# Performance work log

Hardware: AMD Instinct MI355X
Metric: run time of the kernel (lower is better)

The kernel has to match this reference:

```python
import jax, jax.numpy as jnp
import numpy as np
import math

B, S, HID, H, DH = 4, 1024, 1024, 16, 64  # batch, seq, hidden, heads, head_dim


def _rotate_half(x):
    x1, x2 = jnp.split(x, 2, axis=-1)
    return jnp.concatenate([-x2, x1], axis=-1)


def _apply_rope(t, freqs):
    # t: [B,H,S,DH], freqs: [S,rot_dim]; here rot_dim == DH so no pass-through part
    rot = freqs.shape[-1]
    cos_ = jnp.cos(freqs)[None, None, :, :].astype(t.dtype)
    sin_ = jnp.sin(freqs)[None, None, :, :].astype(t.dtype)
    t_rot, t_pass = t[..., :rot], t[..., rot:]
    t_rot = t_rot * cos_ + _rotate_half(t_rot) * sin_
    return jnp.concatenate([t_rot, t_pass], axis=-1)


def setup_inputs() -> dict:
    key = jax.random.key(0)
    ks = jax.random.split(key, 8)
    hidden_states = jax.random.normal(ks[0], (B, S, HID), dtype=jnp.float32)
    # additive mask: valid prefix of random length per batch row, -1e9 on padding
    lengths = jax.random.randint(ks[1], (B,), 3 * S // 4, S + 1)
    pos = jnp.arange(S)
    attention_mask = jnp.where(pos[None, :] < lengths[:, None], 0.0, -1e9)
    attention_mask = attention_mask.astype(jnp.float32)[:, None, None, :]  # [B,1,1,S]
    # rotary frequencies: standard RoPE angles, duplicated halves -> [S, DH]
    inv_freq = 1.0 / (10000.0 ** (jnp.arange(0, DH // 2, dtype=jnp.float32) / (DH // 2)))
    ang = pos.astype(jnp.float32)[:, None] * inv_freq[None, :]
    freqs = jnp.concatenate([ang, ang], axis=-1)  # [S, DH]
    sc = 0.02
    Wq = jax.random.normal(ks[2], (HID, HID), dtype=jnp.float32) * sc
    Wk = jax.random.normal(ks[3], (HID, HID), dtype=jnp.float32) * sc
    Wv = jax.random.normal(ks[4], (HID, HID), dtype=jnp.float32) * sc
    bq = jnp.zeros((HID,), dtype=jnp.float32)
    bk = jnp.zeros((HID,), dtype=jnp.float32)
    bv = jnp.zeros((HID,), dtype=jnp.float32)
    return dict(hidden_states=hidden_states, attention_mask=attention_mask, freqs=freqs,
                Wq=Wq, bq=bq, Wk=Wk, bk=bk, Wv=Wv, bv=bv)


def reference(hidden_states, attention_mask, freqs, Wq, bq, Wk, bk, Wv, bv):
    b, s, _ = hidden_states.shape
    # QKV projections -> [B,H,S,DH]
    q = (hidden_states @ Wq + bq).reshape(b, s, H, DH).transpose(0, 2, 1, 3)
    k = (hidden_states @ Wk + bk).reshape(b, s, H, DH).transpose(0, 2, 1, 3)
    v = (hidden_states @ Wv + bv).reshape(b, s, H, DH).transpose(0, 2, 1, 3)
    # inline RoPE on q and k (same freqs for both, as (rotary_pos_emb,)*2)
    q = _apply_rope(q, freqs)
    k = _apply_rope(k, freqs)
    scores = jnp.einsum('bhqd,bhkd->bhqk', q, k) / math.sqrt(DH)
    scores = scores + attention_mask  # additive mask broadcast over [B,H,S,S]
    probs = jax.nn.softmax(scores, axis=-1)
    # no_prob_mask filtering: zero out masked key columns
    probs = jnp.where(attention_mask < -1e-5, 0.0, probs)
    # dropout prob is 0.0 (eval) -> identity
    ctx = jnp.einsum('bhqk,bhkd->bhqd', probs, v)
    ctx = ctx.transpose(0, 2, 1, 3).reshape(b, s, H * DH)
    return ctx
```

## Files before the change

kernel.cpp:

```cpp
#include <hip/hip_runtime.h>
#include <hip/hip_bf16.h>
#include <cmath>

#define NB   4
#define NS   1024
#define NHID 1024
#define NH   16
#define NDH  64
#define QKV_PLANE (NB * NH * NS * NDH)

typedef __attribute__((ext_vector_type(8))) short bf16x8;
typedef __attribute__((ext_vector_type(4))) float f32x4;

typedef __attribute__((address_space(1))) const void gv_t;
typedef __attribute__((address_space(3))) void       lv_t;

__device__ __forceinline__ void gload16(const void* g, void* l) {
    __builtin_amdgcn_global_load_lds((gv_t*)g, (lv_t*)l, 16, 0, 0);
}

__device__ __forceinline__ unsigned short f2b(float f) {
    union { float f; unsigned int u; } v; v.f = f;
    unsigned int r = (v.u + 0x7fff + ((v.u >> 16) & 1)) >> 16;
    return (unsigned short)r;
}

__device__ __forceinline__ unsigned int f2b2(float a, float b) {
    __hip_bfloat162 h = __float22bfloat162_rn(make_float2(a, b));
    union { __hip_bfloat162 h; unsigned int u; } v; v.h = h;
    return v.u;
}

__device__ __forceinline__ float fexp2(float x) {
#if __has_builtin(__builtin_amdgcn_exp2f)
    return __builtin_amdgcn_exp2f(x);
#else
    return exp2f(x);
#endif
}

__global__ __launch_bounds__(256) void cast_hs_kernel(
    const float* __restrict__ hs, unsigned short* __restrict__ hsb)
{
    const int idx = (blockIdx.x * 256 + threadIdx.x) * 4;
    float4 v = *(const float4*)&hs[idx];
    ushort4 o;
    o.x = f2b(v.x); o.y = f2b(v.y); o.z = f2b(v.z); o.w = f2b(v.w);
    *(ushort4*)&hsb[idx] = o;
}

__global__ __launch_bounds__(256) void wt_prep_kernel(
    const float* __restrict__ Wq, const float* __restrict__ Wk,
    const float* __restrict__ Wv, unsigned short* __restrict__ wt)
{
    const int z = blockIdx.z;
    const float* __restrict__ W = (z == 0) ? Wq : (z == 1) ? Wk : Wv;
    __shared__ float t[64][65];
    const int k0 = blockIdx.x * 64, n0 = blockIdx.y * 64;
    const int tid = threadIdx.x;
    #pragma unroll
    for (int c = 0; c < 16; ++c) {
        const int flat = c * 256 + tid;
        const int r = flat >> 6, cc = flat & 63;
        t[r][cc] = W[(size_t)(k0 + r) * NHID + n0 + cc];
    }
    __syncthreads();
    #pragma unroll
    for (int c = 0; c < 16; ++c) {
        const int flat = c * 256 + tid;
        const int r = flat >> 6, cc = flat & 63;
        wt[(size_t)(z * 1024 + n0 + r) * NHID + k0 + cc] = f2b(t[cc][r]);
    }
}

__global__ __launch_bounds__(256) void fused_gemm_kernel(
    const unsigned short* __restrict__ hsb,
    const unsigned short* __restrict__ wt,
    const float* __restrict__ freqs,
    const float* __restrict__ bq, const float* __restrict__ bk,
    const float* __restrict__ bv,
    unsigned short* __restrict__ qkv)
{
    __shared__ short As[128 * 32];
    __shared__ short Bs[128 * 32];

    const int tid  = threadIdx.x;
    const int lane = tid & 63;
    const int wv   = __builtin_amdgcn_readfirstlane(tid >> 6);
    const bool vmode = (blockIdx.x >= 16);

    const unsigned short* Amat;
    const unsigned short* Bmat;
    int a_base, b_base, m0, n0, vb_ = 0;
    if (!vmode) {
        n0 = blockIdx.x * 128;
        m0 = blockIdx.y * 128;
        Amat = hsb;  a_base = m0;
        Bmat = wt;   b_base = n0;
    } else {
        m0  = (blockIdx.x - 16) * 128;
        vb_ = blockIdx.y >> 3;
        n0  = (blockIdx.y & 7) * 128;
        Amat = wt;   a_base = 2048 + m0;
        Bmat = hsb;  b_base = vb_ * 1024 + n0;
    }

    const int L0 = 2 * wv, L1 = 2 * wv + 1;
    const int r_in = lane >> 2;
    const int kc   = (lane & 3) * 8;
    const unsigned short* gA0 = Amat + (size_t)(a_base + L0 * 16 + r_in) * NHID + kc;
    const unsigned short* gA1 = Amat + (size_t)(a_base + L1 * 16 + r_in) * NHID + kc;
    const unsigned short* gB0 = Bmat + (size_t)(b_base + L0 * 16 + r_in) * NHID + kc;
    const unsigned short* gB1 = Bmat + (size_t)(b_base + L1 * 16 + r_in) * NHID + kc;
    short* lA0 = As + L0 * 512;
    short* lA1 = As + L1 * 512;
    short* lB0 = Bs + L0 * 512;
    short* lB1 = Bs + L1 * 512;

    const int R  = (wv & 1) * 64;
    const int CW = (wv >> 1) * 64;
    const int c0 = lane & 15;
    const int kg = (lane >> 4) * 8;
    int aoff[4], boff[4];
    #pragma unroll
    for (int i = 0; i < 4; ++i) aoff[i] = (R  + 16 * i + c0) * 32 + kg;
    #pragma unroll
    for (int j = 0; j < 4; ++j) boff[j] = (CW + 16 * j + c0) * 32 + kg;

    f32x4 acc[4][4] = {};

    for (int k0 = 0; k0 < NHID; k0 += 32) {
        __syncthreads();
        gload16(gA0 + k0, lA0);
        gload16(gA1 + k0, lA1);
        gload16(gB0 + k0, lB0);
        gload16(gB1 + k0, lB1);
        __syncthreads();
        bf16x8 af[4], bfr[4];
        #pragma unroll
        for (int i = 0; i < 4; ++i) af[i]  = *(const bf16x8*)&As[aoff[i]];
        #pragma unroll
        for (int j = 0; j < 4; ++j) bfr[j] = *(const bf16x8*)&Bs[boff[j]];
        #pragma unroll
        for (int i = 0; i < 4; ++i)
            #pragma unroll
            for (int j = 0; j < 4; ++j)
                acc[i][j] = __builtin_amdgcn_mfma_f32_16x16x32_bf16(
                    af[i], bfr[j], acc[i][j], 0, 0, 0);
    }

    if (!vmode) {
        const int z  = n0 >> 10;
        const int hd = ((n0 & 1023) + CW) >> 6;
        const float* __restrict__ bb = (z == 0) ? bq : bk;
        const float b0 = bb[hd * 64 + c0];
        const float b1 = bb[hd * 64 + c0 + 16];
        const float b2 = bb[hd * 64 + c0 + 32];
        const float b3 = bb[hd * 64 + c0 + 48];
        unsigned short* __restrict__ base = qkv + (size_t)z * QKV_PLANE;
        const int mrow = m0 + R + (lane >> 4) * 4;

        #pragma unroll
        for (int i = 0; i < 4; ++i) {
            #pragma unroll
            for (int r = 0; r < 4; ++r) {
                const int m    = mrow + 16 * i + r;
                const int bidx = m >> 10;
                const int s    = m & 1023;
                float o0 = acc[i][0][r] + b0;
                float o1 = acc[i][1][r] + b1;
                float o2 = acc[i][2][r] + b2;
                float o3 = acc[i][3][r] + b3;
                unsigned short* op = base + (((size_t)bidx * NH + hd) * NS + s) * NDH;
                const float a0 = freqs[s * NDH + c0];
                const float a1 = freqs[s * NDH + c0 + 16];
                float s0, cf0, s1, cf1;
                sincosf(a0, &s0, &cf0);
                sincosf(a1, &s1, &cf1);
                op[c0]      = f2b(o0 * cf0 - o2 * s0);
                op[c0 + 16] = f2b(o1 * cf1 - o3 * s1);
                op[c0 + 32] = f2b(o2 * cf0 + o0 * s0);
                op[c0 + 48] = f2b(o3 * cf1 + o1 * s1);
            }
        }
    } else {
        unsigned short* __restrict__ vplane = qkv + 2 * (size_t)QKV_PLANE;
        const int mrow = m0 + R + (lane >> 4) * 4;
        #pragma unroll
        for (int i = 0; i < 4; ++i) {
            #pragma unroll
            for (int r = 0; r < 4; ++r) {
                const int m = mrow + 16 * i + r;
                const float bvm = bv[m];
                unsigned short* op = vplane + ((size_t)(vb_ * 1024 + m)) * NS + n0 + CW + c0;
                op[0]  = f2b(acc[i][0][r] + bvm);
                op[16] = f2b(acc[i][1][r] + bvm);
                op[32] = f2b(acc[i][2][r] + bvm);
                op[48] = f2b(acc[i][3][r] + bvm);
            }
        }
    }
}

__global__ __launch_bounds__(512) void attn_kernel(
    const unsigned short* __restrict__ qkv, const float* __restrict__ mask,
    float* __restrict__ out)
{
    const int qt = blockIdx.x, h = blockIdx.y, b = blockIdx.z;
    const unsigned short* qp  = qkv + ((size_t)(b * NH + h) * NS) * NDH;
    const unsigned short* kp  = qp + QKV_PLANE;
    const unsigned short* vtp = qkv + 2 * (size_t)QKV_PLANE
                              + ((size_t)(b * NH + h) * NDH) * NS;

    __shared__ unsigned short KsA[64 * 64];
    __shared__ unsigned short VtA[64 * 64];
    __shared__ unsigned short PsA[128 * 64];
    __shared__ float Mk[1024];
    __shared__ float Ll[128];

    const int tid  = threadIdx.x;
    const int lane = tid & 63;
    const int w    = __builtin_amdgcn_readfirstlane(tid >> 6);
    const int c0   = lane & 15;
    const int g    = lane >> 4;
    const int sw7  = c0 & 7;
    const float C1 = 0.125f * 1.44269504f;

    {
        const int i = tid * 2;
        float2 mv = *(const float2*)&mask[(size_t)b * NS + i];
        Mk[i]     = mv.x * 1.44269504f;
        Mk[i + 1] = mv.y * 1.44269504f;
    }

    bf16x8 qf[2];
    #pragma unroll
    for (int ks = 0; ks < 2; ++ks)
        qf[ks] = *(const bf16x8*)&qp[
            (size_t)(qt * 128 + w * 16 + c0) * NDH + g * 8 + ks * 32];

    const int i8 = lane >> 3, c8 = lane & 7;
    const int gsw = (c8 ^ i8) * 8;
    const unsigned short* gk = kp  + (size_t)(w * 8 + i8) * NDH + gsw;
    const unsigned short* gv = vtp + (size_t)(w * 8 + i8) * NS  + gsw;
    unsigned short* lk = KsA + w * 512;
    unsigned short* lv = VtA + w * 512;

    int kaddr[4][2], pw4[4], pr[2];
    #pragma unroll
    for (int mt = 0; mt < 4; ++mt)
        #pragma unroll
        for (int ks = 0; ks < 2; ++ks)
            kaddr[mt][ks] = (mt * 16 + c0) * 64 + ((g + ks * 4) ^ sw7) * 8;
    #pragma unroll
    for (int mt = 0; mt < 4; ++mt)
        pw4[mt] = (w * 16 + c0) * 64 + ((2 * mt + (g >> 1)) ^ sw7) * 8 + (g & 1) * 4;
    #pragma unroll
    for (int ks = 0; ks < 2; ++ks)
        pr[ks] = (w * 16 + c0) * 64 + ((g + ks * 4) ^ sw7) * 8;

    float lrow = 0.f;
    f32x4 O[4] = {};

    for (int kt = 0; kt < 16; ++kt) {
        __syncthreads();
        gload16(gk, lk);
        gload16(gv, lv);
        gk += 64 * NDH;
        gv += 64;
        __syncthreads();

        bf16x8 kf[4][2];
        #pragma unroll
        for (int mt = 0; mt < 4; ++mt)
            #pragma unroll
            for (int ks = 0; ks < 2; ++ks)
                kf[mt][ks] = *(const bf16x8*)&KsA[kaddr[mt][ks]];
        f32x4 S[4];
        #pragma unroll
        for (int mt = 0; mt < 4; ++mt) {
            f32x4 a = {};
            a = __builtin_amdgcn_mfma_f32_16x16x32_bf16(kf[mt][0], qf[0], a, 0, 0, 0);
            a = __builtin_amdgcn_mfma_f32_16x16x32_bf16(kf[mt][1], qf[1], a, 0, 0, 0);
            S[mt] = a;
        }

        float psum = 0.f;
        #pragma unroll
        for (int mt = 0; mt < 4; ++mt) {
            float4 mv = *(const float4*)&Mk[kt * 64 + mt * 16 + g * 4];
            float p0 = fexp2(S[mt][0] * C1 + mv.x);
            float p1 = fexp2(S[mt][1] * C1 + mv.y);
            float p2 = fexp2(S[mt][2] * C1 + mv.z);
            float p3 = fexp2(S[mt][3] * C1 + mv.w);
            psum += (p0 + p1) + (p2 + p3);
            uint2 u;
            u.x = f2b2(p0, p1);
            u.y = f2b2(p2, p3);
            *(uint2*)&PsA[pw4[mt]] = u;
        }
        lrow += psum;

        bf16x8 pf[2], vf[4][2];
        #pragma unroll
        for (int ks = 0; ks < 2; ++ks)
            pf[ks] = *(const bf16x8*)&PsA[pr[ks]];
        #pragma unroll
        for (int nd = 0; nd < 4; ++nd)
            #pragma unroll
            for (int ks = 0; ks < 2; ++ks)
                vf[nd][ks] = *(const bf16x8*)&VtA[kaddr[nd][ks]];
        #pragma unroll
        for (int nd = 0; nd < 4; ++nd) {
            f32x4 o = O[nd];
            o = __builtin_amdgcn_mfma_f32_16x16x32_bf16(pf[0], vf[nd][0], o, 0, 0, 0);
            o = __builtin_amdgcn_mfma_f32_16x16x32_bf16(pf[1], vf[nd][1], o, 0, 0, 0);
            O[nd] = o;
        }
    }

    lrow += __shfl_xor(lrow, 16);
    lrow += __shfl_xor(lrow, 32);
    if (g == 0) Ll[w * 16 + c0] = lrow;
    float4 lv4 = *(const float4*)&Ll[w * 16 + g * 4];
    float inv[4];
    #pragma unroll
    for (int r = 0; r < 4; ++r) inv[r] = 1.0f / ((const float*)&lv4)[r];

    #pragma unroll
    for (int nd = 0; nd < 4; ++nd)
        #pragma unroll
        for (int r = 0; r < 4; ++r) {
            const int row = qt * 128 + w * 16 + g * 4 + r;
            const int col = h * 64 + nd * 16 + c0;
            out[((size_t)b * NS + row) * NHID + col] = O[nd][r] * inv[r];
        }
}

extern "C" void kernel_launch(void* const* d_in, const int* in_sizes, int n_in,
                              void* d_out, int out_size, void* d_ws, size_t ws_size,
                              hipStream_t stream) {
    const float* hs    = (const float*)d_in[0];
    const float* mask  = (const float*)d_in[1];
    const float* freqs = (const float*)d_in[2];
    const float* Wq    = (const float*)d_in[3];
    const float* bq    = (const float*)d_in[4];
    const float* Wk    = (const float*)d_in[5];
    const float* bk    = (const float*)d_in[6];
    const float* Wv    = (const float*)d_in[7];
    const float* bv    = (const float*)d_in[8];
    float* out = (float*)d_out;

    char* ws = (char*)d_ws;
    unsigned short* qkvb = (unsigned short*)ws;
    unsigned short* hsb  = (unsigned short*)(ws + 25165824);
    unsigned short* wtb  = (unsigned short*)(ws + 33554432);

    cast_hs_kernel<<<4096, 256, 0, stream>>>(hs, hsb);
    wt_prep_kernel<<<dim3(16, 16, 3), 256, 0, stream>>>(Wq, Wk, Wv, wtb);
    fused_gemm_kernel<<<dim3(24, 32), 256, 0, stream>>>(hsb, wtb, freqs,
                                                        bq, bk, bv, qkvb);
    attn_kernel<<<dim3(NS / 128, NH, NB), 512, 0, stream>>>(qkvb, mask, out);
}
```

Before: 158.7 us.

## Merge prep kernels, precompute RoPE sin/cos, widen GEMM K-tile, skip masked key tiles

Folds the hidden-state cast and weight transpose into one prep launch that also precomputes a cos/sin table, so the GEMM epilogue no longer calls sincosf per element. The QKV GEMM now stages 64-wide K tiles with an XOR-swizzled LDS layout, halving barrier count per K step and reducing bank conflicts. The attention kernel scans the mask and stops iterating over trailing key tiles that are fully padded. Costs are more LDS per GEMM block and a small extra workspace table; the tile skip relies on the mask having a padded suffix.

```diff
diff --git a/kernel.cpp b/kernel.cpp
--- a/kernel.cpp
+++ b/kernel.cpp
@@ -39,25 +39,44 @@
 #endif
 }
 
-__global__ __launch_bounds__(256) void cast_hs_kernel(
-    const float* __restrict__ hs, unsigned short* __restrict__ hsb)
+__global__ __launch_bounds__(256) void prep_kernel(
+    const float* __restrict__ hs, const float* __restrict__ freqs,
+    const float* __restrict__ Wq, const float* __restrict__ Wk,
+    const float* __restrict__ Wv,
+    unsigned short* __restrict__ hsb, unsigned short* __restrict__ wt,
+    float2* __restrict__ cs)
 {
-    const int idx = (blockIdx.x * 256 + threadIdx.x) * 4;
-    float4 v = *(const float4*)&hs[idx];
-    ushort4 o;
-    o.x = f2b(v.x); o.y = f2b(v.y); o.z = f2b(v.z); o.w = f2b(v.w);
-    *(ushort4*)&hsb[idx] = o;
-}
-
-__global__ __launch_bounds__(256) void wt_prep_kernel(
-    const float* __restrict__ Wq, const float* __restrict__ Wk,
-    const float* __restrict__ Wv, unsigned short* __restrict__ wt)
-{
-    const int z = blockIdx.z;
+    const int z   = blockIdx.z;
+    const int tid = threadIdx.x;
+
+    if (z == 3) {
+        const int bx = blockIdx.y * 16 + blockIdx.x;
+        #pragma unroll
+        for (int c = 0; c < 16; ++c) {
+            const int idx = bx * 16384 + (c * 256 + tid) * 4;
+            float4 v = *(const float4*)&hs[idx];
+            ushort4 o;
+            o.x = f2b(v.x); o.y = f2b(v.y); o.z = f2b(v.z); o.w = f2b(v.w);
+            *(ushort4*)&hsb[idx] = o;
+        }
+        return;
+    }
+    if (z == 4) {
+        const int bx = blockIdx.y * 16 + blockIdx.x;
+        if (bx < 128) {
+            const int id = bx * 256 + tid;
+            const int s = id >> 5, d = id & 31;
+            const float ang = freqs[s * NDH + d];
+            float sn, cn;
+            sincosf(ang, &sn, &cn);
+            cs[id] = make_float2(cn, sn);
+        }
+        return;
+    }
+
     const float* __restrict__ W = (z == 0) ? Wq : (z == 1) ? Wk : Wv;
     __shared__ float t[64][65];
     const int k0 = blockIdx.x * 64, n0 = blockIdx.y * 64;
-    const int tid = threadIdx.x;
     #pragma unroll
     for (int c = 0; c < 16; ++c) {
         const int flat = c * 256 + tid;
@@ -76,13 +95,13 @@
 __global__ __launch_bounds__(256) void fused_gemm_kernel(
     const unsigned short* __restrict__ hsb,
     const unsigned short* __restrict__ wt,
-    const float* __restrict__ freqs,
+    const float2* __restrict__ cs,
     const float* __restrict__ bq, const float* __restrict__ bk,
     const float* __restrict__ bv,
     unsigned short* __restrict__ qkv)
 {
-    __shared__ short As[128 * 32];
-    __shared__ short Bs[128 * 32];
+    __shared__ short As[128 * 64];
+    __shared__ short Bs[128 * 64];
 
     const int tid  = threadIdx.x;
     const int lane = tid & 63;
@@ -105,48 +124,59 @@
         Bmat = hsb;  b_base = vb_ * 1024 + n0;
     }
 
-    const int L0 = 2 * wv, L1 = 2 * wv + 1;
-    const int r_in = lane >> 2;
-    const int kc   = (lane & 3) * 8;
-    const unsigned short* gA0 = Amat + (size_t)(a_base + L0 * 16 + r_in) * NHID + kc;
-    const unsigned short* gA1 = Amat + (size_t)(a_base + L1 * 16 + r_in) * NHID + kc;
-    const unsigned short* gB0 = Bmat + (size_t)(b_base + L0 * 16 + r_in) * NHID + kc;
-    const unsigned short* gB1 = Bmat + (size_t)(b_base + L1 * 16 + r_in) * NHID + kc;
-    short* lA0 = As + L0 * 512;
-    short* lA1 = As + L1 * 512;
-    short* lB0 = Bs + L0 * 512;
-    short* lB1 = Bs + L1 * 512;
+    const int ri  = lane >> 3;
+    const int kcs = ((lane & 7) ^ ri) * 8;
+    const unsigned short* gA[4];
+    const unsigned short* gB[4];
+    short* lA[4];
+    short* lB[4];
+    #pragma unroll
+    for (int j = 0; j < 4; ++j) {
+        const int L = 4 * wv + j;
+        gA[j] = Amat + (size_t)(a_base + L * 8 + ri) * NHID + kcs;
+        gB[j] = Bmat + (size_t)(b_base + L * 8 + ri) * NHID + kcs;
+        lA[j] = As + L * 512;
+        lB[j] = Bs + L * 512;
+    }
 
     const int R  = (wv & 1) * 64;
     const int CW = (wv >> 1) * 64;
     const int c0 = lane & 15;
-    const int kg = (lane >> 4) * 8;
-    int aoff[4], boff[4];
-    #pragma unroll
-    for (int i = 0; i < 4; ++i) aoff[i] = (R  + 16 * i + c0) * 32 + kg;
-    #pragma unroll
-    for (int j = 0; j < 4; ++j) boff[j] = (CW + 16 * j + c0) * 32 + kg;
+    const int g  = lane >> 4;
+    const int sw7 = c0 & 7;
+    int aoff[4][2], boff[4][2];
+    #pragma unroll
+    for (int i = 0; i < 4; ++i)
+        #pragma unroll
+        for (int ks = 0; ks < 2; ++ks) {
+            aoff[i][ks] = (R  + 16 * i + c0) * 64 + ((g + 4 * ks) ^ sw7) * 8;
+            boff[i][ks] = (CW + 16 * i + c0) * 64 + ((g + 4 * ks) ^ sw7) * 8;
+        }
 
     f32x4 acc[4][4] = {};
 
-    for (int k0 = 0; k0 < NHID; k0 += 32) {
+    for (int k0 = 0; k0 < NHID; k0 += 64) {
         __syncthreads();
-        gload16(gA0 + k0, lA0);
-        gload16(gA1 + k0, lA1);
-        gload16(gB0 + k0, lB0);
-        gload16(gB1 + k0, lB1);
+        #pragma unroll
+        for (int j = 0; j < 4; ++j) {
+            gload16(gA[j] + k0, lA[j]);
+            gload16(gB[j] + k0, lB[j]);
+        }
         __syncthreads();
-        bf16x8 af[4], bfr[4];
-        #pragma unroll
-        for (int i = 0; i < 4; ++i) af[i]  = *(const bf16x8*)&As[aoff[i]];
-        #pragma unroll
-        for (int j = 0; j < 4; ++j) bfr[j] = *(const bf16x8*)&Bs[boff[j]];
-        #pragma unroll
-        for (int i = 0; i < 4; ++i)
-            #pragma unroll
-            for (int j = 0; j < 4; ++j)
-                acc[i][j] = __builtin_amdgcn_mfma_f32_16x16x32_bf16(
-                    af[i], bfr[j], acc[i][j], 0, 0, 0);
+        #pragma unroll
+        for (int ks = 0; ks < 2; ++ks) {
+            bf16x8 af[4], bfr[4];
+            #pragma unroll
+            for (int i = 0; i < 4; ++i) af[i]  = *(const bf16x8*)&As[aoff[i][ks]];
+            #pragma unroll
+            for (int j = 0; j < 4; ++j) bfr[j] = *(const bf16x8*)&Bs[boff[j][ks]];
+            #pragma unroll
+            for (int i = 0; i < 4; ++i)
+                #pragma unroll
+                for (int j = 0; j < 4; ++j)
+                    acc[i][j] = __builtin_amdgcn_mfma_f32_16x16x32_bf16(
+                        af[i], bfr[j], acc[i][j], 0, 0, 0);
+        }
     }
 
     if (!vmode) {
@@ -172,15 +202,12 @@
                 float o2 = acc[i][2][r] + b2;
                 float o3 = acc[i][3][r] + b3;
                 unsigned short* op = base + (((size_t)bidx * NH + hd) * NS + s) * NDH;
-                const float a0 = freqs[s * NDH + c0];
-                const float a1 = freqs[s * NDH + c0 + 16];
-                float s0, cf0, s1, cf1;
-                sincosf(a0, &s0, &cf0);
-                sincosf(a1, &s1, &cf1);
-                op[c0]      = f2b(o0 * cf0 - o2 * s0);
-                op[c0 + 16] = f2b(o1 * cf1 - o3 * s1);
-                op[c0 + 32] = f2b(o2 * cf0 + o0 * s0);
-                op[c0 + 48] = f2b(o3 * cf1 + o1 * s1);
+                const float2 cs0 = cs[s * 32 + c0];
+                const float2 cs1 = cs[s * 32 + c0 + 16];
+                op[c0]      = f2b(o0 * cs0.x - o2 * cs0.y);
+                op[c0 + 16] = f2b(o1 * cs1.x - o3 * cs1.y);
+                op[c0 + 32] = f2b(o2 * cs0.x + o0 * cs0.y);
+                op[c0 + 48] = f2b(o3 * cs1.x + o1 * cs1.y);
             }
         }
     } else {
@@ -259,10 +286,14 @@
     for (int ks = 0; ks < 2; ++ks)
         pr[ks] = (w * 16 + c0) * 64 + ((g + ks * 4) ^ sw7) * 8;
 
+    __syncthreads();
+    int ktmax = 16;
+    while (ktmax > 1 && Mk[(ktmax - 1) * 64] < -1.0f) --ktmax;
+
     float lrow = 0.f;
     f32x4 O[4] = {};
 
-    for (int kt = 0; kt < 16; ++kt) {
+    for (int kt = 0; kt < ktmax; ++kt) {
         __syncthreads();
         gload16(gk, lk);
         gload16(gv, lv);
@@ -355,10 +386,11 @@
     unsigned short* qkvb = (unsigned short*)ws;
     unsigned short* hsb  = (unsigned short*)(ws + 25165824);
     unsigned short* wtb  = (unsigned short*)(ws + 33554432);
-
-    cast_hs_kernel<<<4096, 256, 0, stream>>>(hs, hsb);
-    wt_prep_kernel<<<dim3(16, 16, 3), 256, 0, stream>>>(Wq, Wk, Wv, wtb);
-    fused_gemm_kernel<<<dim3(24, 32), 256, 0, stream>>>(hsb, wtb, freqs,
+    float2*         csb  = (float2*)       (ws + 39845888);
+
+    prep_kernel<<<dim3(16, 16, 5), 256, 0, stream>>>(hs, freqs, Wq, Wk, Wv,
+                                                     hsb, wtb, csb);
+    fused_gemm_kernel<<<dim3(24, 32), 256, 0, stream>>>(hsb, wtb, csb,
                                                         bq, bk, bv, qkvb);
     attn_kernel<<<dim3(NS / 128, NH, NB), 512, 0, stream>>>(qkvb, mask, out);
 }
```

New measurement: 157.7 us. No clear change (-0.6%).
